# Performance work log

Hardware: AMD Instinct MI355X
Metric: run time of the kernel (lower is better)

Reference implementation:

```python
import jax, jax.numpy as jnp
import numpy as np

N_NODES = 100_000
N_EDGES = 1_600_000
IN_DIM = 128
HIDDEN = 128
OUT_DIM = 64
N_LAYERS = 8
ALPHA = 0.1  # GCN2Conv alpha; beta = 1.0 since theta/layer not given


def setup_inputs() -> dict:
    key = jax.random.key(0)
    ks = jax.random.split(key, 6)
    x = jax.random.normal(ks[0], (N_NODES, IN_DIM), dtype=jnp.float32)
    edge_index = jax.random.randint(ks[1], (2, N_EDGES), 0, N_NODES, dtype=jnp.int64)
    W_in = jax.random.normal(ks[2], (IN_DIM, HIDDEN), dtype=jnp.float32) / np.sqrt(IN_DIM)
    b_in = jnp.zeros((HIDDEN,), jnp.float32)
    conv_w = jax.random.normal(ks[3], (N_LAYERS, HIDDEN, HIDDEN), dtype=jnp.float32) / np.sqrt(HIDDEN)
    W_out = jax.random.normal(ks[4], (HIDDEN, OUT_DIM), dtype=jnp.float32) / np.sqrt(HIDDEN)
    b_out = jnp.zeros((OUT_DIM,), jnp.float32)
    return {"x": x, "edge_index": edge_index, "W_in": W_in, "b_in": b_in,
            "conv_w": conv_w, "W_out": W_out, "b_out": b_out}


def reference(x, edge_index, W_in, b_in, conv_w, W_out, b_out):
    N = x.shape[0]
    # gcn_norm with self-loops: A_hat = D^-1/2 (A + I) D^-1/2
    loops = jnp.arange(N, dtype=edge_index.dtype)
    ei = jnp.concatenate([edge_index, jnp.stack([loops, loops])], axis=1)
    row, col = ei[0], ei[1]  # source, target
    deg = jax.ops.segment_sum(jnp.ones(ei.shape[1], x.dtype), col, num_segments=N)
    dinv = jnp.where(deg > 0, jax.lax.rsqrt(deg), 0.0)
    norm = dinv[row] * dinv[col]  # [E+N]

    h = jax.nn.relu(x @ W_in + b_in)  # input projection
    x0 = h  # initial residual
    for l in range(conv_w.shape[0]):
        # sparse neighbor aggregation: out[i] = sum_{(j->i)} norm * h[j]
        agg = jax.ops.segment_sum(h[row] * norm[:, None], col, num_segments=N)
        support = (1.0 - ALPHA) * agg + ALPHA * x0  # initial residual mix
        h = jax.nn.relu(support @ conv_w[l])  # beta=1 -> out = support @ W
        # dropout: identity in eval mode
    return h @ W_out + b_out
```

## Files before the change

kernel.cpp:

```cpp
#include <hip/hip_runtime.h>
#include <hip/hip_fp16.h>
#include <cstdint>
#include <cstddef>


#define HID 128

using f16x8 = __attribute__((ext_vector_type(8))) _Float16;
using f32x4 = __attribute__((ext_vector_type(4))) float;


__global__ void k_hist(const int* __restrict__ col, int E, int* __restrict__ cnt) {
  int e = blockIdx.x * blockDim.x + threadIdx.x;
  if (e < E) atomicAdd(&cnt[col[e]], 1);
}

__global__ __launch_bounds__(256) void k_blocksum_dinv(const int* __restrict__ cnt,
                                                       int* __restrict__ bsum,
                                                       float* __restrict__ dinv, int N) {
  __shared__ int s[256];
  int t = threadIdx.x;
  int i = blockIdx.x * 256 + t;
  int v = (i < N) ? cnt[i] : 0;
  if (i < N) dinv[i] = rsqrtf((float)v + 1.0f);
  s[t] = v;
  __syncthreads();
  for (int off = 128; off > 0; off >>= 1) {
    if (t < off) s[t] += s[t + off];
    __syncthreads();
  }
  if (t == 0) bsum[blockIdx.x] = s[0];
}

__global__ __launch_bounds__(512) void k_scan_bsum(const int* __restrict__ bsum,
                                                   int* __restrict__ bofs, int nb) {
  __shared__ int s[512];
  __shared__ int carry;
  int t = threadIdx.x;
  if (t == 0) carry = 0;
  __syncthreads();
  for (int base = 0; base < nb; base += 512) {
    int i = base + t;
    int v = (i < nb) ? bsum[i] : 0;
    s[t] = v;
    __syncthreads();
    for (int off = 1; off < 512; off <<= 1) {
      int a = (t >= off) ? s[t - off] : 0;
      __syncthreads();
      s[t] += a;
      __syncthreads();
    }
    if (i < nb) bofs[i] = carry + s[t] - v;
    __syncthreads();
    if (t == 0) carry += s[511];
    __syncthreads();
  }
}

__global__ __launch_bounds__(256) void k_scan_write(const int* __restrict__ cnt,
                                                    const int* __restrict__ bofs,
                                                    int* __restrict__ row_ptr, int N) {
  __shared__ int s[256];
  int t = threadIdx.x;
  int i = blockIdx.x * 256 + t;
  int v = (i < N) ? cnt[i] : 0;
  s[t] = v;
  __syncthreads();
  for (int off = 1; off < 256; off <<= 1) {
    int a = (t >= off) ? s[t - off] : 0;
    __syncthreads();
    s[t] += a;
    __syncthreads();
  }
  int excl = bofs[blockIdx.x] + s[t] - v;
  if (i < N) row_ptr[i] = excl;
  if (i == N - 1) row_ptr[N] = excl + v;
}

__global__ void k_fill(const int* __restrict__ row, const int* __restrict__ col, int E,
                       const int* __restrict__ row_ptr, int* __restrict__ fill,
                       int* __restrict__ csr_src) {
  int e = blockIdx.x * blockDim.x + threadIdx.x;
  if (e >= E) return;
  int r = row[e], c = col[e];
  int p = row_ptr[c] + atomicAdd(&fill[c], 1);
  csr_src[p] = r;
}

__global__ void k_wprep(const float* __restrict__ Wc, const float* __restrict__ W_in,
                        const float* __restrict__ W_out, _Float16* __restrict__ Wt,
                        int L) {
  int id = blockIdx.x * blockDim.x + threadIdx.x;
  int nl = L * 16384;
  if (id < nl) {
    int l = id >> 14, r = id & 16383;
    int k = r >> 7, n = r & 127;
    Wt[(size_t)l * 16384 + n * 128 + k] = (_Float16)Wc[(size_t)l * 16384 + k * 128 + n];
  } else if (id < nl + 16384) {
    int r = id - nl;
    int k = r >> 7, n = r & 127;
    Wt[(size_t)nl + n * 128 + k] = (_Float16)W_in[k * 128 + n];
  } else if (id < nl + 16384 + 8192) {
    int r = id - nl - 16384;
    int k = r >> 6, n = r & 63;
    Wt[(size_t)(nl + 16384) + n * 128 + k] = (_Float16)W_out[k * 64 + n];
  }
}

__global__ void k_f2h(const float* __restrict__ src, _Float16* __restrict__ dst, int n) {
  int i = (blockIdx.x * blockDim.x + threadIdx.x) * 4;
  if (i < n) {
    float4 v = *(const float4*)(src + i);
    dst[i] = (_Float16)v.x;
    dst[i + 1] = (_Float16)v.y;
    dst[i + 2] = (_Float16)v.z;
    dst[i + 3] = (_Float16)v.w;
  }
}


__global__ __launch_bounds__(256) void k_aggregate16(
    const _Float16* __restrict__ hp, const _Float16* __restrict__ x0h,
    const float* __restrict__ dinv, const int* __restrict__ row_ptr,
    const int* __restrict__ csr_src, _Float16* __restrict__ support, int N) {
  const __half* h = (const __half*)hp;
  int node = blockIdx.x * 4 + (threadIdx.x >> 6);
  if (node >= N) return;
  int lane = threadIdx.x & 63;
  int beg = row_ptr[node], end = row_ptr[node + 1];
  float di = dinv[node];
  float2 f0 = __half22float2(((const __half2*)(h + (size_t)node * HID))[lane]);
  float ax = di * f0.x;
  float ay = di * f0.y;
  int j = beg;
  for (; j + 4 <= end; j += 4) {
    int s0 = csr_src[j], s1 = csr_src[j + 1], s2 = csr_src[j + 2], s3 = csr_src[j + 3];
    float w0 = dinv[s0], w1 = dinv[s1], w2 = dinv[s2], w3 = dinv[s3];
    __half2 a0 = ((const __half2*)(h + (size_t)s0 * HID))[lane];
    __half2 a1 = ((const __half2*)(h + (size_t)s1 * HID))[lane];
    __half2 a2 = ((const __half2*)(h + (size_t)s2 * HID))[lane];
    __half2 a3 = ((const __half2*)(h + (size_t)s3 * HID))[lane];
    float2 f;
    f = __half22float2(a0); ax = fmaf(w0, f.x, ax); ay = fmaf(w0, f.y, ay);
    f = __half22float2(a1); ax = fmaf(w1, f.x, ax); ay = fmaf(w1, f.y, ay);
    f = __half22float2(a2); ax = fmaf(w2, f.x, ax); ay = fmaf(w2, f.y, ay);
    f = __half22float2(a3); ax = fmaf(w3, f.x, ax); ay = fmaf(w3, f.y, ay);
  }
  for (; j < end; ++j) {
    int s = csr_src[j];
    float w = dinv[s];
    float2 f = __half22float2(((const __half2*)(h + (size_t)s * HID))[lane]);
    ax = fmaf(w, f.x, ax);
    ay = fmaf(w, f.y, ay);
  }
  float2 xv = __half22float2(((const __half2*)((const __half*)x0h + (size_t)node * HID))[lane]);
  float s9 = 0.9f * di;
  float ox = s9 * ax + 0.1f * xv.x;
  float oy = s9 * ay + 0.1f * xv.y;
  ((__half2*)support)[(size_t)node * (HID / 2) + lane] = __floats2half2_rn(ox, oy);
}


template <int NC, bool RELU, bool BIAS, bool OHALF>
__global__ __launch_bounds__(256) void k_mfma_gemm(const _Float16* __restrict__ A,
                                                   const _Float16* __restrict__ Bt,
                                                   const float* __restrict__ bias,
                                                   void* __restrict__ Cv, int M) {
  constexpr int NT = NC / 16;
  int tid = threadIdx.x;
  int w = tid >> 6, l = tid & 63;
  int lm = l & 15, kg = l >> 4;
  int row0 = blockIdx.x * 128 + w * 32;

  f32x4 acc[2][NT];
#pragma unroll
  for (int mt = 0; mt < 2; ++mt)
#pragma unroll
    for (int nt = 0; nt < NT; ++nt) acc[mt][nt] = (f32x4){0.f, 0.f, 0.f, 0.f};

#pragma unroll
  for (int ks = 0; ks < 128; ks += 32) {
    f16x8 a0 = *(const f16x8*)(A + (size_t)(row0 + lm) * 128 + ks + kg * 8);
    f16x8 a1 = *(const f16x8*)(A + (size_t)(row0 + 16 + lm) * 128 + ks + kg * 8);
#pragma unroll
    for (int nt = 0; nt < NT; ++nt) {
      f16x8 b = *(const f16x8*)(Bt + (size_t)(nt * 16 + lm) * 128 + ks + kg * 8);
      acc[0][nt] = __builtin_amdgcn_mfma_f32_16x16x32_f16(a0, b, acc[0][nt], 0, 0, 0);
      acc[1][nt] = __builtin_amdgcn_mfma_f32_16x16x32_f16(a1, b, acc[1][nt], 0, 0, 0);
    }
  }

#pragma unroll
  for (int mt = 0; mt < 2; ++mt) {
#pragma unroll
    for (int nt = 0; nt < NT; ++nt) {
      int colc = nt * 16 + lm;
      float bv = BIAS ? bias[colc] : 0.0f;
#pragma unroll
      for (int i = 0; i < 4; ++i) {
        int r = row0 + mt * 16 + kg * 4 + i;
        if (r >= M) continue;
        float v = acc[mt][nt][i] + bv;
        if (RELU) v = fmaxf(v, 0.0f);
        if (OHALF)
          ((_Float16*)Cv)[(size_t)r * NC + colc] = (_Float16)v;
        else
          ((float*)Cv)[(size_t)r * NC + colc] = v;
      }
    }
  }
}


extern "C" void kernel_launch(void* const* d_in, const int* in_sizes, int n_in,
                              void* d_out, int out_size, void* d_ws, size_t ws_size,
                              hipStream_t stream) {
  const float* x     = (const float*)d_in[0];
  const int*   ei    = (const int*)d_in[1];
  const float* W_in  = (const float*)d_in[2];
  const float* b_in  = (const float*)d_in[3];
  const float* Wc    = (const float*)d_in[4];
  const float* W_out = (const float*)d_in[5];
  const float* b_out = (const float*)d_in[6];
  float* out = (float*)d_out;

  const int N = in_sizes[0] / HID;
  const int E = in_sizes[1] / 2;
  const int L = in_sizes[4] / (HID * HID);
  const int nb = (N + 255) / 256;
  const int* row = ei;
  const int* col = ei + E;

  char* p = (char*)d_ws;
  auto alloc = [&](size_t bytes) {
    char* q = p;
    p += (bytes + 255) & ~(size_t)255;
    return q;
  };
  _Float16* x0h   = (_Float16*)alloc((size_t)N * HID * 2);
  _Float16* sup16 = (_Float16*)alloc((size_t)N * HID * 2);
  _Float16* h16   = (_Float16*)alloc((size_t)N * HID * 2);
  _Float16* Wt    = (_Float16*)alloc((size_t)(L * 16384 + 16384 + 8192) * 2);
  int*    cnt     = (int*)alloc((size_t)N * 4);
  int*    row_ptr = (int*)alloc((size_t)(N + 1) * 4);
  int*    fill    = (int*)alloc((size_t)N * 4);
  int*    bsum    = (int*)alloc((size_t)nb * 4);
  int*    bofs    = (int*)alloc((size_t)nb * 4);
  float*  dinv    = (float*)alloc((size_t)N * 4);
  int*    csr_src = (int*)alloc((size_t)E * 4);
  (void)ws_size; (void)n_in; (void)out_size;

  const _Float16* Wt_in  = Wt + (size_t)L * 16384;
  const _Float16* Wt_out = Wt + (size_t)L * 16384 + 16384;

  hipMemsetAsync(cnt, 0, (size_t)N * 4, stream);
  hipMemsetAsync(fill, 0, (size_t)N * 4, stream);

  int nw = L * 16384 + 16384 + 8192;
  k_wprep<<<(nw + 255) / 256, 256, 0, stream>>>(Wc, W_in, W_out, Wt, L);
  k_hist<<<(E + 255) / 256, 256, 0, stream>>>(col, E, cnt);
  k_blocksum_dinv<<<nb, 256, 0, stream>>>(cnt, bsum, dinv, N);
  k_scan_bsum<<<1, 512, 0, stream>>>(bsum, bofs, nb);
  k_scan_write<<<nb, 256, 0, stream>>>(cnt, bofs, row_ptr, N);
  k_fill<<<(E + 255) / 256, 256, 0, stream>>>(row, col, E, row_ptr, fill, csr_src);

  int ggrid = (N + 127) / 128;
  k_f2h<<<(N * HID / 4 + 255) / 256, 256, 0, stream>>>(x, sup16, N * HID);
  k_mfma_gemm<128, true, true, true><<<ggrid, 256, 0, stream>>>(sup16, Wt_in, b_in,
                                                                x0h, N);

  const _Float16* hin = x0h;
  for (int l = 0; l < L; ++l) {
    k_aggregate16<<<(N + 3) / 4, 256, 0, stream>>>(hin, x0h, dinv, row_ptr, csr_src,
                                                   sup16, N);
    k_mfma_gemm<128, true, false, true><<<ggrid, 256, 0, stream>>>(
        sup16, Wt + (size_t)l * 16384, nullptr, h16, N);
    hin = h16;
  }
  k_mfma_gemm<64, false, true, false><<<ggrid, 256, 0, stream>>>(hin, Wt_out, b_out,
                                                                 out, N);
}
```

Measured before the change: 1.054 ms.

## Two-pass bucketed CSR build, fuse input fp32 cast into GEMM, unroll aggregation

CSR construction now runs in two passes: edges are first bucketed by destination block of 128 nodes into a temporary int2 buffer, then scattered per node, so the final scatter writes land in more local memory regions. The separate fp32-to-fp16 conversion kernel is removed and the input GEMM reads fp32 directly and converts in registers. The aggregation loop is unrolled to 8 neighbors with gathers issued before the dinv loads, to raise memory-level parallelism. GEMM row indices are clamped to M-1, which avoids out-of-bounds reads on the last tile. The cost is an extra pass and an extra E*8-byte temporary buffer for the CSR build.

```diff
diff --git a/kernel.cpp b/kernel.cpp
--- a/kernel.cpp
+++ b/kernel.cpp
@@ -5,6 +5,7 @@
 
 
 #define HID 128
+#define BSHIFT 7
 
 using f16x8 = __attribute__((ext_vector_type(8))) _Float16;
 using f32x4 = __attribute__((ext_vector_type(4))) float;
@@ -77,14 +78,25 @@
   if (i == N - 1) row_ptr[N] = excl + v;
 }
 
-__global__ void k_fill(const int* __restrict__ row, const int* __restrict__ col, int E,
-                       const int* __restrict__ row_ptr, int* __restrict__ fill,
-                       int* __restrict__ csr_src) {
+__global__ void k_scatterA(const int* __restrict__ row, const int* __restrict__ col,
+                           int E, const int* __restrict__ row_ptr,
+                           int* __restrict__ bfill, int2* __restrict__ tmp) {
   int e = blockIdx.x * blockDim.x + threadIdx.x;
   if (e >= E) return;
   int r = row[e], c = col[e];
-  int p = row_ptr[c] + atomicAdd(&fill[c], 1);
-  csr_src[p] = r;
+  int b = c >> BSHIFT;
+  int p = row_ptr[b << BSHIFT] + atomicAdd(&bfill[b], 1);
+  tmp[p] = make_int2(r, c);
+}
+
+__global__ void k_scatterB(const int2* __restrict__ tmp, int E,
+                           const int* __restrict__ row_ptr, int* __restrict__ fill,
+                           int* __restrict__ csr_src) {
+  int i = blockIdx.x * blockDim.x + threadIdx.x;
+  if (i >= E) return;
+  int2 t = tmp[i];
+  int p = row_ptr[t.y] + atomicAdd(&fill[t.y], 1);
+  csr_src[p] = t.x;
 }
 
 __global__ void k_wprep(const float* __restrict__ Wc, const float* __restrict__ W_in,
@@ -107,17 +119,6 @@
   }
 }
 
-__global__ void k_f2h(const float* __restrict__ src, _Float16* __restrict__ dst, int n) {
-  int i = (blockIdx.x * blockDim.x + threadIdx.x) * 4;
-  if (i < n) {
-    float4 v = *(const float4*)(src + i);
-    dst[i] = (_Float16)v.x;
-    dst[i + 1] = (_Float16)v.y;
-    dst[i + 2] = (_Float16)v.z;
-    dst[i + 3] = (_Float16)v.w;
-  }
-}
-
 
 __global__ __launch_bounds__(256) void k_aggregate16(
     const _Float16* __restrict__ hp, const _Float16* __restrict__ x0h,
@@ -133,18 +134,42 @@
   float ax = di * f0.x;
   float ay = di * f0.y;
   int j = beg;
-  for (; j + 4 <= end; j += 4) {
-    int s0 = csr_src[j], s1 = csr_src[j + 1], s2 = csr_src[j + 2], s3 = csr_src[j + 3];
-    float w0 = dinv[s0], w1 = dinv[s1], w2 = dinv[s2], w3 = dinv[s3];
+  for (; j + 8 <= end; j += 8) {
+    int s0 = csr_src[j],     s1 = csr_src[j + 1], s2 = csr_src[j + 2], s3 = csr_src[j + 3];
+    int s4 = csr_src[j + 4], s5 = csr_src[j + 5], s6 = csr_src[j + 6], s7 = csr_src[j + 7];
     __half2 a0 = ((const __half2*)(h + (size_t)s0 * HID))[lane];
     __half2 a1 = ((const __half2*)(h + (size_t)s1 * HID))[lane];
     __half2 a2 = ((const __half2*)(h + (size_t)s2 * HID))[lane];
     __half2 a3 = ((const __half2*)(h + (size_t)s3 * HID))[lane];
+    __half2 a4 = ((const __half2*)(h + (size_t)s4 * HID))[lane];
+    __half2 a5 = ((const __half2*)(h + (size_t)s5 * HID))[lane];
+    __half2 a6 = ((const __half2*)(h + (size_t)s6 * HID))[lane];
+    __half2 a7 = ((const __half2*)(h + (size_t)s7 * HID))[lane];
+    float w0 = dinv[s0], w1 = dinv[s1], w2 = dinv[s2], w3 = dinv[s3];
+    float w4 = dinv[s4], w5 = dinv[s5], w6 = dinv[s6], w7 = dinv[s7];
     float2 f;
     f = __half22float2(a0); ax = fmaf(w0, f.x, ax); ay = fmaf(w0, f.y, ay);
     f = __half22float2(a1); ax = fmaf(w1, f.x, ax); ay = fmaf(w1, f.y, ay);
     f = __half22float2(a2); ax = fmaf(w2, f.x, ax); ay = fmaf(w2, f.y, ay);
     f = __half22float2(a3); ax = fmaf(w3, f.x, ax); ay = fmaf(w3, f.y, ay);
+    f = __half22float2(a4); ax = fmaf(w4, f.x, ax); ay = fmaf(w4, f.y, ay);
+    f = __half22float2(a5); ax = fmaf(w5, f.x, ax); ay = fmaf(w5, f.y, ay);
+    f = __half22float2(a6); ax = fmaf(w6, f.x, ax); ay = fmaf(w6, f.y, ay);
+    f = __half22float2(a7); ax = fmaf(w7, f.x, ax); ay = fmaf(w7, f.y, ay);
+  }
+  if (j + 4 <= end) {
+    int s0 = csr_src[j], s1 = csr_src[j + 1], s2 = csr_src[j + 2], s3 = csr_src[j + 3];
+    __half2 a0 = ((const __half2*)(h + (size_t)s0 * HID))[lane];
+    __half2 a1 = ((const __half2*)(h + (size_t)s1 * HID))[lane];
+    __half2 a2 = ((const __half2*)(h + (size_t)s2 * HID))[lane];
+    __half2 a3 = ((const __half2*)(h + (size_t)s3 * HID))[lane];
+    float w0 = dinv[s0], w1 = dinv[s1], w2 = dinv[s2], w3 = dinv[s3];
+    float2 f;
+    f = __half22float2(a0); ax = fmaf(w0, f.x, ax); ay = fmaf(w0, f.y, ay);
+    f = __half22float2(a1); ax = fmaf(w1, f.x, ax); ay = fmaf(w1, f.y, ay);
+    f = __half22float2(a2); ax = fmaf(w2, f.x, ax); ay = fmaf(w2, f.y, ay);
+    f = __half22float2(a3); ax = fmaf(w3, f.x, ax); ay = fmaf(w3, f.y, ay);
+    j += 4;
   }
   for (; j < end; ++j) {
     int s = csr_src[j];
@@ -161,8 +186,8 @@
 }
 
 
-template <int NC, bool RELU, bool BIAS, bool OHALF>
-__global__ __launch_bounds__(256) void k_mfma_gemm(const _Float16* __restrict__ A,
+template <int NC, bool RELU, bool BIAS, bool AF32, bool OHALF>
+__global__ __launch_bounds__(256) void k_mfma_gemm(const void* __restrict__ Av,
                                                    const _Float16* __restrict__ Bt,
                                                    const float* __restrict__ bias,
                                                    void* __restrict__ Cv, int M) {
@@ -171,6 +196,8 @@
   int w = tid >> 6, l = tid & 63;
   int lm = l & 15, kg = l >> 4;
   int row0 = blockIdx.x * 128 + w * 32;
+  int r0 = min(row0 + lm, M - 1);
+  int r1 = min(row0 + 16 + lm, M - 1);
 
   f32x4 acc[2][NT];
 #pragma unroll
@@ -180,8 +207,22 @@
 
 #pragma unroll
   for (int ks = 0; ks < 128; ks += 32) {
-    f16x8 a0 = *(const f16x8*)(A + (size_t)(row0 + lm) * 128 + ks + kg * 8);
-    f16x8 a1 = *(const f16x8*)(A + (size_t)(row0 + 16 + lm) * 128 + ks + kg * 8);
+    f16x8 a0, a1;
+    if (AF32) {
+      const float* Af = (const float*)Av;
+      float4 p0 = *(const float4*)(Af + (size_t)r0 * 128 + ks + kg * 8);
+      float4 p1 = *(const float4*)(Af + (size_t)r0 * 128 + ks + kg * 8 + 4);
+      float4 q0 = *(const float4*)(Af + (size_t)r1 * 128 + ks + kg * 8);
+      float4 q1 = *(const float4*)(Af + (size_t)r1 * 128 + ks + kg * 8 + 4);
+      a0[0] = (_Float16)p0.x; a0[1] = (_Float16)p0.y; a0[2] = (_Float16)p0.z; a0[3] = (_Float16)p0.w;
+      a0[4] = (_Float16)p1.x; a0[5] = (_Float16)p1.y; a0[6] = (_Float16)p1.z; a0[7] = (_Float16)p1.w;
+      a1[0] = (_Float16)q0.x; a1[1] = (_Float16)q0.y; a1[2] = (_Float16)q0.z; a1[3] = (_Float16)q0.w;
+      a1[4] = (_Float16)q1.x; a1[5] = (_Float16)q1.y; a1[6] = (_Float16)q1.z; a1[7] = (_Float16)q1.w;
+    } else {
+      const _Float16* Ah = (const _Float16*)Av;
+      a0 = *(const f16x8*)(Ah + (size_t)r0 * 128 + ks + kg * 8);
+      a1 = *(const f16x8*)(Ah + (size_t)r1 * 128 + ks + kg * 8);
+    }
 #pragma unroll
     for (int nt = 0; nt < NT; ++nt) {
       f16x8 b = *(const f16x8*)(Bt + (size_t)(nt * 16 + lm) * 128 + ks + kg * 8);
@@ -228,6 +269,7 @@
   const int E = in_sizes[1] / 2;
   const int L = in_sizes[4] / (HID * HID);
   const int nb = (N + 255) / 256;
+  const int nbk = (N + (1 << BSHIFT) - 1) >> BSHIFT;
   const int* row = ei;
   const int* col = ei + E;
 
@@ -244,10 +286,12 @@
   int*    cnt     = (int*)alloc((size_t)N * 4);
   int*    row_ptr = (int*)alloc((size_t)(N + 1) * 4);
   int*    fill    = (int*)alloc((size_t)N * 4);
+  int*    bfill   = (int*)alloc((size_t)nbk * 4);
   int*    bsum    = (int*)alloc((size_t)nb * 4);
   int*    bofs    = (int*)alloc((size_t)nb * 4);
   float*  dinv    = (float*)alloc((size_t)N * 4);
   int*    csr_src = (int*)alloc((size_t)E * 4);
+  int2*   tmp     = (int2*)alloc((size_t)E * 8);
   (void)ws_size; (void)n_in; (void)out_size;
 
   const _Float16* Wt_in  = Wt + (size_t)L * 16384;
@@ -255,6 +299,7 @@
 
   hipMemsetAsync(cnt, 0, (size_t)N * 4, stream);
   hipMemsetAsync(fill, 0, (size_t)N * 4, stream);
+  hipMemsetAsync(bfill, 0, (size_t)nbk * 4, stream);
 
   int nw = L * 16384 + 16384 + 8192;
   k_wprep<<<(nw + 255) / 256, 256, 0, stream>>>(Wc, W_in, W_out, Wt, L);
@@ -262,21 +307,21 @@
   k_blocksum_dinv<<<nb, 256, 0, stream>>>(cnt, bsum, dinv, N);
   k_scan_bsum<<<1, 512, 0, stream>>>(bsum, bofs, nb);
   k_scan_write<<<nb, 256, 0, stream>>>(cnt, bofs, row_ptr, N);
-  k_fill<<<(E + 255) / 256, 256, 0, stream>>>(row, col, E, row_ptr, fill, csr_src);
+  k_scatterA<<<(E + 255) / 256, 256, 0, stream>>>(row, col, E, row_ptr, bfill, tmp);
+  k_scatterB<<<(E + 255) / 256, 256, 0, stream>>>(tmp, E, row_ptr, fill, csr_src);
 
   int ggrid = (N + 127) / 128;
-  k_f2h<<<(N * HID / 4 + 255) / 256, 256, 0, stream>>>(x, sup16, N * HID);
-  k_mfma_gemm<128, true, true, true><<<ggrid, 256, 0, stream>>>(sup16, Wt_in, b_in,
-                                                                x0h, N);
+  k_mfma_gemm<128, true, true, true, true><<<ggrid, 256, 0, stream>>>(x, Wt_in, b_in,
+                                                                      x0h, N);
 
   const _Float16* hin = x0h;
   for (int l = 0; l < L; ++l) {
     k_aggregate16<<<(N + 3) / 4, 256, 0, stream>>>(hin, x0h, dinv, row_ptr, csr_src,
                                                    sup16, N);
-    k_mfma_gemm<128, true, false, true><<<ggrid, 256, 0, stream>>>(
+    k_mfma_gemm<128, true, false, false, true><<<ggrid, 256, 0, stream>>>(
         sup16, Wt + (size_t)l * 16384, nullptr, h16, N);
     hin = h16;
   }
-  k_mfma_gemm<64, false, true, false><<<ggrid, 256, 0, stream>>>(hin, Wt_out, b_out,
-                                                                 out, N);
-}
+  k_mfma_gemm<64, false, true, false, false><<<ggrid, 256, 0, stream>>>(hin, Wt_out,
+                                                                        b_out, out, N);
+}
```

Result: slower. 1.318 ms (+25.0%).
